# Kernel optimization log

Hardware: AMD Instinct MI355X
Metric: run time of the kernel (lower is better)

Reference implementation:

```python
import jax, jax.numpy as jnp
import numpy as np

NEG = -1e10

def setup_inputs() -> dict:
    key = jax.random.key(0)
    ks = jax.random.split(key, 12)
    B, W, V, D, R, VOCAB = 16, 64, 64, 256, 64, 50000
    head_ctx = jax.random.randint(ks[0], (B, W), 0, VOCAB)
    tail_ctx = jax.random.randint(ks[1], (B, V), 0, VOCAB)
    emb = jax.random.normal(ks[2], (VOCAB, D), dtype=jnp.float32) * 0.02
    rela_mat = jax.random.normal(ks[3], (R, D), dtype=jnp.float32) * 0.02
    fc_w = jax.random.normal(ks[4], (3 * D, D), dtype=jnp.float32) * (1.0 / np.sqrt(3 * D))
    fc_b = jnp.zeros((D,), jnp.float32)
    att_w1 = jax.random.normal(ks[5], (D, D), dtype=jnp.float32) * (1.0 / np.sqrt(D))
    att_b1 = jnp.zeros((D,), jnp.float32)
    att_w2 = jax.random.normal(ks[6], (D, 1), dtype=jnp.float32) * (1.0 / np.sqrt(D))
    att_b2 = jnp.zeros((1,), jnp.float32)
    out_w = jax.random.normal(ks[7], (D, 1), dtype=jnp.float32) * (1.0 / np.sqrt(D))
    out_b = jnp.zeros((1,), jnp.float32)
    return {"head_ctx": head_ctx, "tail_ctx": tail_ctx, "emb": emb, "rela_mat": rela_mat,
            "fc_w": fc_w, "fc_b": fc_b, "att_w1": att_w1, "att_b1": att_b1,
            "att_w2": att_w2, "att_b2": att_b2, "out_w": out_w, "out_b": out_b}

def reference(head_ctx, tail_ctx, emb, rela_mat, fc_w, fc_b, att_w1, att_b1, att_w2, att_b2, out_w, out_b):
    A = emb[head_ctx]            # [B, W, D]
    Bt = emb[tail_ctx]           # [B, V, D]
    Bsz, W, D = A.shape
    V = Bt.shape[1]
    R = rela_mat.shape[0]
    N = W * V
    # DistMult scoring for every (head_i, tail_j, rela_r) triple, no repeat materialization
    scores = jnp.einsum('bid,bjd,rd->bijr', A, Bt, rela_mat).reshape(Bsz, N, R)
    # cut_rela_score: mask relations not beating the null (last) relation
    null = scores[:, :, -1:]
    scores = jnp.where(scores <= null, NEG, scores)
    norm_scores = jax.nn.softmax(scores, axis=-1)            # [B, N, R]
    rela_vec = jnp.einsum('bnr,rd->bnd', norm_scores, rela_mat)
    # tuple (i,j) pairing: index n = i*V + j
    A_rep = jnp.broadcast_to(A[:, :, None, :], (Bsz, W, V, D)).reshape(Bsz, N, D)
    B_rep = jnp.broadcast_to(Bt[:, None, :, :], (Bsz, W, V, D)).reshape(Bsz, N, D)
    tuple_vec = jnp.tanh(jnp.concatenate([A_rep, B_rep, rela_vec], axis=-1) @ fc_w + fc_b)  # [B, N, D]
    # tuple attention pooling
    att = jnp.tanh(tuple_vec @ att_w1 + att_b1) @ att_w2 + att_b2   # [B, N, 1]
    att_norms = jax.nn.softmax(att, axis=1)                          # [B, N, 1]
    fuse = jnp.sum(att_norms * tuple_vec, axis=1)                    # [B, D]
    logits = (fuse @ out_w + out_b).squeeze(-1)                      # [B]
    return logits, att_norms, norm_scores
```

## Files before the change

### kernel.cpp

```cpp
#include <hip/hip_runtime.h>
#include <hip/hip_bf16.h>

#define NB 16
#define NW 64
#define NV 64
#define ND 256
#define NR 64
#define NN 4096
#define NEGV -10000000000.0f

typedef __attribute__((ext_vector_type(8))) short short8;
typedef __attribute__((ext_vector_type(4))) float f32x4;

__device__ inline float cvt(const void* p, int idx, int flag) {
  if (flag) return __bfloat162float(((const __hip_bfloat16*)p)[idx]);
  return ((const float*)p)[idx];
}
__device__ inline void stv(void* p, int idx, float v, int flag) {
  if (flag) ((__hip_bfloat16*)p)[idx] = __float2bfloat16(v);
  else ((float*)p)[idx] = v;
}
__device__ inline float bf2f(short s) {
  return __uint_as_float(((unsigned int)(unsigned short)s) << 16);
}
__device__ inline float tanh_fast(float x) {
  float ax = fabsf(x);
  float e = __expf(-2.f * ax);
  float r = (1.f - e) / (1.f + e);
  return copysignf(r, x);
}

__global__ void k_detect(const unsigned int* embw, int* flagp) {
  __shared__ float red[256];
  int t = threadIdx.x;
  float mx = 0.f;
  for (int i = t; i < 1024; i += 256) {
    unsigned int w = embw[i];
    unsigned int fb = (w & 0xffffu) << 16;
    float a = fabsf(__uint_as_float(fb));
    if (!(a < 1e9f)) a = 1e9f;
    mx = fmaxf(mx, a);
  }
  red[t] = mx;
  __syncthreads();
  for (int s = 128; s > 0; s >>= 1) {
    if (t < s) red[t] = fmaxf(red[t], red[t + s]);
    __syncthreads();
  }
  if (t == 0) flagp[0] = (red[0] < 1000.f) ? 1 : 0;
}

__global__ void k_prep(const void* rela, float* relaT,
                       const void* b1, const void* w2, const void* outw,
                       const void* b2, const void* outb, float* sp,
                       const void* w1, __hip_bfloat16* w1b,
                       const int* head, const int* tail, const void* emb,
                       float* Af, float* Bf, const int* flagp) {
  int flag = flagp[0];
  int blk = blockIdx.x;
  int t = threadIdx.x;
  if (blk < 64) {
    relaT[t * NR + blk] = cvt(rela, blk * ND + t, flag);
  } else if (blk == 64) {
    sp[t] = cvt(b1, t, flag);
    sp[256 + t] = cvt(w2, t, flag);
    sp[512 + t] = cvt(outw, t, flag);
    if (t == 0) {
      sp[768] = cvt(b2, 0, flag);
      sp[769] = cvt(outb, 0, flag);
    }
  } else if (blk < 321) {
    int flat = (blk - 65) * 256 + t;
    int i = flat & 7;
    int lane = (flat >> 3) & 63;
    int kst = (flat >> 9) & 7;
    int nt = flat >> 12;
    int k = kst * 32 + (lane >> 4) * 8 + i;
    int n = nt * 16 + (lane & 15);
    w1b[flat] = __float2bfloat16(cvt(w1, k * ND + n, flag));
  } else {
    int row = blk - 321;
    if (row < NB * NW) {
      int ix = head[row];
      Af[row * ND + t] = cvt(emb, ix * ND + t, flag);
    } else {
      int rr = row - NB * NW;
      int ix = tail[rr];
      Bf[rr * ND + t] = cvt(emb, ix * ND + t, flag);
    }
  }
}

__global__ void k_premm(const float* Af, const float* Bf, const void* rela,
                        const void* fcw, const void* fcb,
                        float* Ah, float* Bh, float* RW, const int* flagp) {
  int flag = flagp[0];
  int row = blockIdx.x;
  int t = threadIdx.x;
  __shared__ float rl[ND];
  float* dst;
  int wbase, addb = 0;
  if (row < 1024) {
    rl[t] = Af[row * ND + t];
    wbase = 0; dst = Ah + row * ND; addb = 1;
  } else if (row < 2048) {
    int rr = row - 1024;
    rl[t] = Bf[rr * ND + t];
    wbase = ND; dst = Bh + rr * ND;
  } else {
    int rr = row - 2048;
    rl[t] = cvt(rela, rr * ND + t, flag);
    wbase = 2 * ND; dst = RW + rr * ND;
  }
  __syncthreads();
  float a0 = 0.f, a1 = 0.f, a2 = 0.f, a3 = 0.f;
  for (int k = 0; k < ND; k += 4) {
    a0 += rl[k]     * cvt(fcw, (wbase + k) * ND + t, flag);
    a1 += rl[k + 1] * cvt(fcw, (wbase + k + 1) * ND + t, flag);
    a2 += rl[k + 2] * cvt(fcw, (wbase + k + 2) * ND + t, flag);
    a3 += rl[k + 3] * cvt(fcw, (wbase + k + 3) * ND + t, flag);
  }
  float acc = (a0 + a1) + (a2 + a3);
  if (addb) acc += cvt(fcb, t, flag);
  dst[t] = acc;
}

__global__ void __launch_bounds__(256) k_scores(const float* Af, const float* Bf,
                                                const float* relaT, void* out,
                                                const int* flagp) {
  int flag = flagp[0];
  int bi = blockIdx.x;
  int b = bi >> 6;
  int t = threadIdx.x;
  int r = t & 63;
  int q = t >> 6;
  __shared__ float Al[ND];
  __shared__ float Bl[4 * ND];
  __shared__ float part[4 * 256];
  Al[t] = Af[bi * ND + t];
  __syncthreads();
  float preR[64];
#pragma unroll
  for (int i2 = 0; i2 < 64; ++i2) {
    int d = q * 64 + i2;
    preR[i2] = Al[d] * relaT[d * NR + r];
  }
  for (int jg = 0; jg < 16; ++jg) {
#pragma unroll
    for (int jj = 0; jj < 4; ++jj)
      Bl[jj * ND + t] = Bf[(b * NV + jg * 4 + jj) * ND + t];
    __syncthreads();
#pragma unroll
    for (int jj = 0; jj < 4; ++jj) {
      float acc = 0.f;
#pragma unroll
      for (int i2 = 0; i2 < 64; ++i2)
        acc += preR[i2] * Bl[jj * ND + q * 64 + i2];
      part[jj * 256 + t] = acc;
    }
    __syncthreads();
    {
      int j4 = q;
      float s = part[j4 * 256 + r] + part[j4 * 256 + 64 + r]
              + part[j4 * 256 + 128 + r] + part[j4 * 256 + 192 + r];
      float nullv = __shfl(s, 63, 64);
      float m = (s <= nullv) ? NEGV : s;
      float mx = m;
#pragma unroll
      for (int o = 32; o > 0; o >>= 1) mx = fmaxf(mx, __shfl_xor(mx, o, 64));
      float e = __expf(m - mx);
      float sum = e;
#pragma unroll
      for (int o = 32; o > 0; o >>= 1) sum += __shfl_xor(sum, o, 64);
      float ns = e / sum;
      int j = jg * 4 + j4;
      int nidx = (bi * 64 + j) * 64 + r;
      stv(out, 16 + NB * NN + nidx, ns, flag);
    }
    __syncthreads();
  }
}

__global__ void __launch_bounds__(256) k_tuple(const float* Ah, const float* Bh,
                                               const float* RW, const void* out,
                                               __hip_bfloat16* tup,
                                               const int* flagp) {
  int flag = flagp[0];
  int bi = blockIdx.x;
  int b = bi >> 6;
  int t = threadIdx.x;
  __shared__ float nsl[4][NR];
  float RWc[64];
#pragma unroll
  for (int rr = 0; rr < 64; ++rr) RWc[rr] = RW[rr * ND + t];
  float base0 = Ah[bi * ND + t];
  int nsbase = 16 + NB * NN + bi * 64 * 64;
  for (int jg = 0; jg < 16; ++jg) {
    nsl[t >> 6][t & 63] = cvt(out, nsbase + (jg * 4 + (t >> 6)) * 64 + (t & 63), flag);
    __syncthreads();
#pragma unroll
    for (int jj = 0; jj < 4; ++jj) {
      int j = jg * 4 + jj;
      float acc = base0 + Bh[(b * NV + j) * ND + t];
#pragma unroll
      for (int rr = 0; rr < 64; ++rr) acc += nsl[jj][rr] * RWc[rr];
      tup[((size_t)bi * 64 + j) * ND + t] = __float2bfloat16(tanh_fast(acc));
    }
    __syncthreads();
  }
}

__global__ void __launch_bounds__(256) k_att2(const __hip_bfloat16* tup,
                                              const __hip_bfloat16* w1b,
                                              const float* sp,
                                              float* att_raw, float* dotv) {
  int t = threadIdx.x;
  int wv = t >> 6, lane = t & 63;
  int r0 = blockIdx.x * 128 + wv * 32;
  const short* tupS = (const short*)tup;
  const short* w1S = (const short*)w1b;
  const float* owf = sp + 512;
  float b2v = sp[768];

  f32x4 acc0[16], acc1[16];
#pragma unroll
  for (int i = 0; i < 16; ++i) {
    acc0[i] = (f32x4){0.f, 0.f, 0.f, 0.f};
    acc1[i] = (f32x4){0.f, 0.f, 0.f, 0.f};
  }
  float dp0 = 0.f, dp1 = 0.f;
  int arow0 = r0 + (lane & 15);
  int arow1 = arow0 + 16;
  int kgrp = lane >> 4;

#pragma unroll
  for (int ks = 0; ks < 8; ++ks) {
    int k0 = ks * 32 + kgrp * 8;
    short8 a0 = *(const short8*)(tupS + (size_t)arow0 * ND + k0);
    short8 a1 = *(const short8*)(tupS + (size_t)arow1 * ND + k0);
#pragma unroll
    for (int i = 0; i < 8; ++i) {
      float w = owf[k0 + i];
      dp0 += bf2f(a0[i]) * w;
      dp1 += bf2f(a1[i]) * w;
    }
#pragma unroll
    for (int nt = 0; nt < 16; ++nt) {
      short8 bfr = *(const short8*)(w1S + (((nt * 8 + ks) * 64 + lane) << 3));
      acc0[nt] = __builtin_amdgcn_mfma_f32_16x16x32_bf16(a0, bfr, acc0[nt], 0, 0, 0);
      acc1[nt] = __builtin_amdgcn_mfma_f32_16x16x32_bf16(a1, bfr, acc1[nt], 0, 0, 0);
    }
  }

  dp0 += __shfl_xor(dp0, 16, 64); dp0 += __shfl_xor(dp0, 32, 64);
  dp1 += __shfl_xor(dp1, 16, 64); dp1 += __shfl_xor(dp1, 32, 64);
  if (lane < 16) {
    dotv[r0 + lane] = dp0;
    dotv[r0 + 16 + lane] = dp1;
  }

  float p0[4] = {0.f, 0.f, 0.f, 0.f};
  float p1[4] = {0.f, 0.f, 0.f, 0.f};
#pragma unroll
  for (int nt = 0; nt < 16; ++nt) {
    int col = nt * 16 + (lane & 15);
    float b1v = sp[col];
    float w2v = sp[256 + col];
#pragma unroll
    for (int reg = 0; reg < 4; ++reg) {
      p0[reg] += tanh_fast(acc0[nt][reg] + b1v) * w2v;
      p1[reg] += tanh_fast(acc1[nt][reg] + b1v) * w2v;
    }
  }
#pragma unroll
  for (int o = 1; o < 16; o <<= 1) {
#pragma unroll
    for (int reg = 0; reg < 4; ++reg) {
      p0[reg] += __shfl_xor(p0[reg], o, 64);
      p1[reg] += __shfl_xor(p1[reg], o, 64);
    }
  }
  if ((lane & 15) == 0) {
    int rb = r0 + (lane >> 4) * 4;
#pragma unroll
    for (int reg = 0; reg < 4; ++reg) {
      att_raw[rb + reg] = p0[reg] + b2v;
      att_raw[rb + 16 + reg] = p1[reg] + b2v;
    }
  }
}

__global__ void k_fuse(const float* att_raw, const float* dotv,
                       const float* sp, void* out, const int* flagp) {
  int flag = flagp[0];
  int b = blockIdx.x;
  int t = threadIdx.x;
  __shared__ float red[256];
  float vals[16];
  float mx = -3.4e38f;
#pragma unroll
  for (int c = 0; c < 16; ++c) {
    vals[c] = att_raw[b * NN + c * 256 + t];
    mx = fmaxf(mx, vals[c]);
  }
  red[t] = mx;
  __syncthreads();
  for (int s = 128; s > 0; s >>= 1) {
    if (t < s) red[t] = fmaxf(red[t], red[t + s]);
    __syncthreads();
  }
  float M = red[0];
  __syncthreads();
  float sm = 0.f;
#pragma unroll
  for (int c = 0; c < 16; ++c) {
    vals[c] = __expf(vals[c] - M);
    sm += vals[c];
  }
  red[t] = sm;
  __syncthreads();
  for (int s = 128; s > 0; s >>= 1) {
    if (t < s) red[t] += red[t + s];
    __syncthreads();
  }
  float Z = red[0];
  __syncthreads();
  float acc = 0.f;
#pragma unroll
  for (int c = 0; c < 16; ++c) {
    int n = c * 256 + t;
    float a = vals[c] / Z;
    stv(out, 16 + b * NN + n, a, flag);
    acc += a * dotv[b * NN + n];
  }
  red[t] = acc;
  __syncthreads();
  for (int s = 128; s > 0; s >>= 1) {
    if (t < s) red[t] += red[t + s];
    __syncthreads();
  }
  if (t == 0) stv(out, b, red[0] + sp[769], flag);
}

extern "C" void kernel_launch(void* const* d_in, const int* in_sizes, int n_in,
                              void* d_out, int out_size, void* d_ws, size_t ws_size,
                              hipStream_t stream) {
  const int* head = (const int*)d_in[0];
  const int* tail = (const int*)d_in[1];
  const void* emb = d_in[2];
  const void* rela = d_in[3];
  const void* fcw = d_in[4];
  const void* fcb = d_in[5];
  const void* w1 = d_in[6];
  const void* b1 = d_in[7];
  const void* w2 = d_in[8];
  const void* b2 = d_in[9];
  const void* outw = d_in[10];
  const void* outb = d_in[11];

  float* ws = (float*)d_ws;
  int* flagp = (int*)d_ws;
  const size_t O_RELAT = 16;
  const size_t O_AF = O_RELAT + 16384;
  const size_t O_BF = O_AF + 262144;
  const size_t O_AH = O_BF + 262144;
  const size_t O_BH = O_AH + 262144;
  const size_t O_RW = O_BH + 262144;
  const size_t O_ATTR = O_RW + 16384;
  const size_t O_DOT = O_ATTR + 65536;
  const size_t O_SP = O_DOT + 65536;
  const size_t O_W1B = O_SP + 1024;
  const size_t O_TUP = O_W1B + 32768;

  float* relaT = ws + O_RELAT;
  float* Af = ws + O_AF;
  float* Bf = ws + O_BF;
  float* Ah = ws + O_AH;
  float* Bh = ws + O_BH;
  float* RW = ws + O_RW;
  float* attr = ws + O_ATTR;
  float* dotv = ws + O_DOT;
  float* sp = ws + O_SP;
  __hip_bfloat16* w1b = (__hip_bfloat16*)(ws + O_W1B);
  __hip_bfloat16* tup = (__hip_bfloat16*)(ws + O_TUP);

  hipLaunchKernelGGL(k_detect, dim3(1), dim3(256), 0, stream,
                     (const unsigned int*)emb, flagp);
  hipLaunchKernelGGL(k_prep, dim3(2369), dim3(256), 0, stream,
                     rela, relaT, b1, w2, outw, b2, outb, sp,
                     w1, w1b, head, tail, emb, Af, Bf, flagp);
  hipLaunchKernelGGL(k_premm, dim3(2112), dim3(256), 0, stream,
                     Af, Bf, rela, fcw, fcb, Ah, Bh, RW, flagp);
  hipLaunchKernelGGL(k_scores, dim3(1024), dim3(256), 0, stream,
                     Af, Bf, relaT, d_out, flagp);
  hipLaunchKernelGGL(k_tuple, dim3(1024), dim3(256), 0, stream,
                     Ah, Bh, RW, d_out, tup, flagp);
  hipLaunchKernelGGL(k_att2, dim3(512), dim3(256), 0, stream,
                     tup, w1b, sp, attr, dotv);
  hipLaunchKernelGGL(k_fuse, dim3(16), dim3(256), 0, stream,
                     attr, dotv, sp, d_out, flagp);
}
```

Measured before the change: 288.2 us.

## Move tuple relation projection to bf16 MFMA and batch premm rows

```diff
diff --git a/kernel.cpp b/kernel.cpp
--- a/kernel.cpp
+++ b/kernel.cpp
@@ -91,42 +91,62 @@
   }
 }
 
-__global__ void k_premm(const float* Af, const float* Bf, const void* rela,
-                        const void* fcw, const void* fcb,
-                        float* Ah, float* Bh, float* RW, const int* flagp) {
+__global__ void __launch_bounds__(256) k_premm(const float* Af, const float* Bf,
+                                               const void* rela, const void* fcw,
+                                               const void* fcb, float* Ah,
+                                               float* Bh, __hip_bfloat16* rwb,
+                                               const int* flagp) {
   int flag = flagp[0];
-  int row = blockIdx.x;
-  int t = threadIdx.x;
-  __shared__ float rl[ND];
-  float* dst;
-  int wbase, addb = 0;
-  if (row < 1024) {
-    rl[t] = Af[row * ND + t];
-    wbase = 0; dst = Ah + row * ND; addb = 1;
-  } else if (row < 2048) {
-    int rr = row - 1024;
-    rl[t] = Bf[rr * ND + t];
-    wbase = ND; dst = Bh + rr * ND;
+  int blk = blockIdx.x;
+  int t = threadIdx.x;
+  __shared__ float rl[4][ND];
+  int base, wbase, addb = 0, isr = 0;
+  const float* src = Af;
+  if (blk < 256) { base = blk * 4; wbase = 0; addb = 1; }
+  else if (blk < 512) { base = (blk - 256) * 4; src = Bf; wbase = ND; }
+  else { base = (blk - 512) * 4; wbase = 2 * ND; isr = 1; }
+#pragma unroll
+  for (int i = 0; i < 4; ++i)
+    rl[i][t] = isr ? cvt(rela, (base + i) * ND + t, flag)
+                   : src[(base + i) * ND + t];
+  __syncthreads();
+  float acc0 = 0.f, acc1 = 0.f, acc2 = 0.f, acc3 = 0.f;
+  const f32x4* r0p = (const f32x4*)rl[0];
+  const f32x4* r1p = (const f32x4*)rl[1];
+  const f32x4* r2p = (const f32x4*)rl[2];
+  const f32x4* r3p = (const f32x4*)rl[3];
+  for (int k4 = 0; k4 < 64; ++k4) {
+    float w0 = cvt(fcw, (wbase + k4 * 4 + 0) * ND + t, flag);
+    float w1v = cvt(fcw, (wbase + k4 * 4 + 1) * ND + t, flag);
+    float w2v = cvt(fcw, (wbase + k4 * 4 + 2) * ND + t, flag);
+    float w3v = cvt(fcw, (wbase + k4 * 4 + 3) * ND + t, flag);
+    f32x4 r0 = r0p[k4], r1 = r1p[k4], r2 = r2p[k4], r3 = r3p[k4];
+    acc0 += r0.x * w0 + r0.y * w1v + r0.z * w2v + r0.w * w3v;
+    acc1 += r1.x * w0 + r1.y * w1v + r1.z * w2v + r1.w * w3v;
+    acc2 += r2.x * w0 + r2.y * w1v + r2.z * w2v + r2.w * w3v;
+    acc3 += r3.x * w0 + r3.y * w1v + r3.z * w2v + r3.w * w3v;
+  }
+  float bias = addb ? cvt(fcb, t, flag) : 0.f;
+  float res[4] = {acc0 + bias, acc1 + bias, acc2 + bias, acc3 + bias};
+  if (!isr) {
+    float* dst = addb ? Ah : Bh;
+#pragma unroll
+    for (int i = 0; i < 4; ++i) dst[(base + i) * ND + t] = res[i];
   } else {
-    int rr = row - 2048;
-    rl[t] = cvt(rela, rr * ND + t, flag);
-    wbase = 2 * ND; dst = RW + rr * ND;
-  }
-  __syncthreads();
-  float a0 = 0.f, a1 = 0.f, a2 = 0.f, a3 = 0.f;
-  for (int k = 0; k < ND; k += 4) {
-    a0 += rl[k]     * cvt(fcw, (wbase + k) * ND + t, flag);
-    a1 += rl[k + 1] * cvt(fcw, (wbase + k + 1) * ND + t, flag);
-    a2 += rl[k + 2] * cvt(fcw, (wbase + k + 2) * ND + t, flag);
-    a3 += rl[k + 3] * cvt(fcw, (wbase + k + 3) * ND + t, flag);
-  }
-  float acc = (a0 + a1) + (a2 + a3);
-  if (addb) acc += cvt(fcb, t, flag);
-  dst[t] = acc;
+#pragma unroll
+    for (int i = 0; i < 4; ++i) {
+      int rr = base + i;
+      int ks = rr >> 5, ii = rr & 7, lh = (rr >> 3) & 3;
+      int nt = t >> 4, ll = t & 15;
+      int flat = ((nt * 2 + ks) * 64 + lh * 16 + ll) * 8 + ii;
+      rwb[flat] = __float2bfloat16(res[i]);
+    }
+  }
 }
 
 __global__ void __launch_bounds__(256) k_scores(const float* Af, const float* Bf,
                                                 const float* relaT, void* out,
+                                                __hip_bfloat16* nsb,
                                                 const int* flagp) {
   int flag = flagp[0];
   int bi = blockIdx.x;
@@ -145,6 +165,7 @@
     int d = q * 64 + i2;
     preR[i2] = Al[d] * relaT[d * NR + r];
   }
+  const f32x4* Bl4 = (const f32x4*)Bl;
   for (int jg = 0; jg < 16; ++jg) {
 #pragma unroll
     for (int jj = 0; jj < 4; ++jj)
@@ -153,9 +174,15 @@
 #pragma unroll
     for (int jj = 0; jj < 4; ++jj) {
       float acc = 0.f;
-#pragma unroll
-      for (int i2 = 0; i2 < 64; ++i2)
-        acc += preR[i2] * Bl[jj * ND + q * 64 + i2];
+      int ib = jj * 64 + q * 16;
+#pragma unroll
+      for (int i4 = 0; i4 < 16; ++i4) {
+        f32x4 bv = Bl4[ib + i4];
+        acc += preR[i4 * 4 + 0] * bv.x;
+        acc += preR[i4 * 4 + 1] * bv.y;
+        acc += preR[i4 * 4 + 2] * bv.z;
+        acc += preR[i4 * 4 + 3] * bv.w;
+      }
       part[jj * 256 + t] = acc;
     }
     __syncthreads();
@@ -176,37 +203,49 @@
       int j = jg * 4 + j4;
       int nidx = (bi * 64 + j) * 64 + r;
       stv(out, 16 + NB * NN + nidx, ns, flag);
-    }
-    __syncthreads();
-  }
-}
-
-__global__ void __launch_bounds__(256) k_tuple(const float* Ah, const float* Bh,
-                                               const float* RW, const void* out,
-                                               __hip_bfloat16* tup,
-                                               const int* flagp) {
-  int flag = flagp[0];
+      nsb[nidx] = __float2bfloat16(ns);
+    }
+    __syncthreads();
+  }
+}
+
+__global__ void __launch_bounds__(256) k_tuple2(const __hip_bfloat16* nsb,
+                                                const __hip_bfloat16* rwb,
+                                                const float* Ah, const float* Bh,
+                                                __hip_bfloat16* tup) {
+  int t = threadIdx.x;
+  int wv = t >> 6, lane = t & 63;
   int bi = blockIdx.x;
   int b = bi >> 6;
-  int t = threadIdx.x;
-  __shared__ float nsl[4][NR];
-  float RWc[64];
-#pragma unroll
-  for (int rr = 0; rr < 64; ++rr) RWc[rr] = RW[rr * ND + t];
-  float base0 = Ah[bi * ND + t];
-  int nsbase = 16 + NB * NN + bi * 64 * 64;
-  for (int jg = 0; jg < 16; ++jg) {
-    nsl[t >> 6][t & 63] = cvt(out, nsbase + (jg * 4 + (t >> 6)) * 64 + (t & 63), flag);
-    __syncthreads();
-#pragma unroll
-    for (int jj = 0; jj < 4; ++jj) {
-      int j = jg * 4 + jj;
-      float acc = base0 + Bh[(b * NV + j) * ND + t];
-#pragma unroll
-      for (int rr = 0; rr < 64; ++rr) acc += nsl[jj][rr] * RWc[rr];
-      tup[((size_t)bi * 64 + j) * ND + t] = __float2bfloat16(tanh_fast(acc));
-    }
-    __syncthreads();
+  const short* nsS = (const short*)nsb;
+  const short* rwS = (const short*)rwb;
+  int m = lane & 15;
+  int kgrp = lane >> 4;
+  f32x4 acc[16];
+#pragma unroll
+  for (int i = 0; i < 16; ++i) acc[i] = (f32x4){0.f, 0.f, 0.f, 0.f};
+  int nrow = bi * 64 + wv * 16 + m;
+#pragma unroll
+  for (int ks = 0; ks < 2; ++ks) {
+    short8 a = *(const short8*)(nsS + (size_t)nrow * 64 + ks * 32 + kgrp * 8);
+#pragma unroll
+    for (int nt = 0; nt < 16; ++nt) {
+      short8 bfr = *(const short8*)(rwS + (((nt * 2 + ks) * 64 + lane) << 3));
+      acc[nt] = __builtin_amdgcn_mfma_f32_16x16x32_bf16(a, bfr, acc[nt], 0, 0, 0);
+    }
+  }
+  int rbase = bi * 64 + wv * 16 + (lane >> 4) * 4;
+  int jbase = rbase & 63;
+#pragma unroll
+  for (int nt = 0; nt < 16; ++nt) {
+    int col = nt * 16 + m;
+    float ahv = Ah[bi * ND + col];
+#pragma unroll
+    for (int reg = 0; reg < 4; ++reg) {
+      int ng = rbase + reg;
+      float v = acc[nt][reg] + ahv + Bh[(size_t)(b * 64 + jbase + reg) * ND + col];
+      tup[(size_t)ng * ND + col] = __float2bfloat16(tanh_fast(v));
+    }
   }
 }
 
@@ -365,23 +404,25 @@
   const size_t O_BF = O_AF + 262144;
   const size_t O_AH = O_BF + 262144;
   const size_t O_BH = O_AH + 262144;
-  const size_t O_RW = O_BH + 262144;
-  const size_t O_ATTR = O_RW + 16384;
+  const size_t O_ATTR = O_BH + 262144;
   const size_t O_DOT = O_ATTR + 65536;
   const size_t O_SP = O_DOT + 65536;
   const size_t O_W1B = O_SP + 1024;
-  const size_t O_TUP = O_W1B + 32768;
+  const size_t O_RWB = O_W1B + 32768;
+  const size_t O_NSB = O_RWB + 8192;
+  const size_t O_TUP = O_NSB + 2097152;
 
   float* relaT = ws + O_RELAT;
   float* Af = ws + O_AF;
   float* Bf = ws + O_BF;
   float* Ah = ws + O_AH;
   float* Bh = ws + O_BH;
-  float* RW = ws + O_RW;
   float* attr = ws + O_ATTR;
   float* dotv = ws + O_DOT;
   float* sp = ws + O_SP;
   __hip_bfloat16* w1b = (__hip_bfloat16*)(ws + O_W1B);
+  __hip_bfloat16* rwb = (__hip_bfloat16*)(ws + O_RWB);
+  __hip_bfloat16* nsb = (__hip_bfloat16*)(ws + O_NSB);
   __hip_bfloat16* tup = (__hip_bfloat16*)(ws + O_TUP);
 
   hipLaunchKernelGGL(k_detect, dim3(1), dim3(256), 0, stream,
@@ -389,12 +430,12 @@
   hipLaunchKernelGGL(k_prep, dim3(2369), dim3(256), 0, stream,
                      rela, relaT, b1, w2, outw, b2, outb, sp,
                      w1, w1b, head, tail, emb, Af, Bf, flagp);
-  hipLaunchKernelGGL(k_premm, dim3(2112), dim3(256), 0, stream,
-                     Af, Bf, rela, fcw, fcb, Ah, Bh, RW, flagp);
+  hipLaunchKernelGGL(k_premm, dim3(528), dim3(256), 0, stream,
+                     Af, Bf, rela, fcw, fcb, Ah, Bh, rwb, flagp);
   hipLaunchKernelGGL(k_scores, dim3(1024), dim3(256), 0, stream,
-                     Af, Bf, relaT, d_out, flagp);
-  hipLaunchKernelGGL(k_tuple, dim3(1024), dim3(256), 0, stream,
-                     Ah, Bh, RW, d_out, tup, flagp);
+                     Af, Bf, relaT, d_out, nsb, flagp);
+  hipLaunchKernelGGL(k_tuple2, dim3(1024), dim3(256), 0, stream,
+                     nsb, rwb, Ah, Bh, tup);
   hipLaunchKernelGGL(k_att2, dim3(512), dim3(256), 0, stream,
                      tup, w1b, sp, attr, dotv);
   hipLaunchKernelGGL(k_fuse, dim3(16), dim3(256), 0, stream,
```

Result: faster. 265.2 us (-8.0%).
